# Optimization experiments

Measured on AMD Instinct MI355X. Metric: run time of the kernel, lower is better.

The kernel has to match this reference:

```python
import jax, jax.numpy as jnp
import numpy as np

TEMPERATURE = 0.5
EPS = 1e-8  # F.cosine_similarity eps


def _neg_mask_indices(B):
    # mask: ones, zero diagonal, zero the two positive off-diagonals
    N = 2 * B
    mask = np.ones((N, N), dtype=bool)
    np.fill_diagonal(mask, False)
    idx = np.arange(B)
    mask[idx, idx + B] = False
    mask[idx + B, idx] = False
    rows, cols = np.nonzero(mask)  # static, computed at trace time
    return rows, cols


def setup_inputs() -> dict:
    key = jax.random.key(0)
    k1, k2 = jax.random.split(key)
    B, D = 4096, 128
    z_i = jax.random.normal(k1, (B, D), dtype=jnp.float32)
    z_j = jax.random.normal(k2, (B, D), dtype=jnp.float32)
    return {"z_i": z_i, "z_j": z_j}


def reference(z_i, z_j):
    B = z_i.shape[0]
    N = 2 * B
    z = jnp.concatenate([z_i, z_j], axis=0)  # [N, D]
    norm = jnp.maximum(jnp.linalg.norm(z, axis=1, keepdims=True), EPS)
    zn = z / norm
    sim = (zn @ zn.T) / TEMPERATURE  # [N, N] cosine similarity / temp

    # positives: the i <-> i+B pairs
    sim_i_j = jnp.diagonal(sim, offset=B)
    sim_j_i = jnp.diagonal(sim, offset=-B)
    positives = jnp.concatenate([sim_i_j, sim_j_i], axis=0)[:, None]  # [N, 1]

    rows, cols = _neg_mask_indices(B)
    negatives = sim[rows, cols].reshape(N, N - 2)  # [N, N-2]

    logits = jnp.concatenate([positives, negatives], axis=1)  # [N, N-1]
    # cross-entropy with labels == 0 (positive is column 0)
    loss = jnp.mean(jax.nn.logsumexp(logits, axis=1) - logits[:, 0])
    return loss
```

## Files before the change

### kernel.cpp

```cpp
#include <hip/hip_runtime.h>
#include <hip/hip_bf16.h>
#include <math.h>


typedef __attribute__((ext_vector_type(8))) short bf16x8;
typedef __attribute__((ext_vector_type(4))) float f32x4;

#define NROWS 8192
#define DDIM  128
#define BHALF 4096
#define CHUNK 32
#define TILE  128
#define NT    64
#define NBLK  2080
#define CPAD  128
#define SQRT_E2S 1.6986435980707531f
#define TWO_LN2  1.3862943611198906f
#define LN2      0.6931471805599453f
#define EXPDIAG  7.38905609893065f

static __device__ __forceinline__ unsigned short f2bf(float f) {
  unsigned int u = __float_as_uint(f);
  unsigned int r = (u + 0x7fffu + ((u >> 16) & 1u)) >> 16;
  return (unsigned short)r;
}

static __device__ __forceinline__ void glds16(const unsigned short* g, unsigned short* l) {
  __builtin_amdgcn_global_load_lds((const __attribute__((address_space(1))) unsigned int*)g,
                                   (__attribute__((address_space(3))) unsigned int*)l,
                                   16, 0, 0);
}

__global__ void norm_kernel(const float* __restrict__ zi, const float* __restrict__ zj,
                            unsigned short* __restrict__ zn,
                            float* __restrict__ pos, float* __restrict__ out) {
  __shared__ float2 xbuf[2][64];
  int wave = threadIdx.x >> 6;
  int lane = threadIdx.x & 63;
  int pi   = blockIdx.x * 2 + (wave & 1);
  int row  = pi + (wave >> 1) * BHALF;
  const float* src = (row < BHALF) ? (zi + (size_t)row * DDIM)
                                   : (zj + (size_t)(row - BHALF) * DDIM);
  float2 v = *(const float2*)(src + 2 * lane);
  float ss = v.x * v.x + v.y * v.y;
  #pragma unroll
  for (int off = 1; off < 64; off <<= 1) ss += __shfl_xor(ss, off);
  float scale = SQRT_E2S / fmaxf(sqrtf(ss), 1e-8f);
  v.x *= scale; v.y *= scale;
  unsigned int lo = f2bf(v.x), hi = f2bf(v.y);
  ((unsigned int*)(zn + (size_t)row * DDIM))[lane] = lo | (hi << 16);

  if (wave >= 2) xbuf[wave - 2][lane] = v;
  __syncthreads();
  if (wave < 2) {
    float2 w = xbuf[wave][lane];
    float d = v.x * w.x + v.y * w.y;
    #pragma unroll
    for (int off = 1; off < 64; off <<= 1) d += __shfl_xor(d, off);
    if (lane == 0) pos[pi] = d;
  }
  if (blockIdx.x == 0 && threadIdx.x == 0) out[0] = 0.0f;
}

__global__ __launch_bounds__(256, 2)
void sim_kernel(const unsigned short* __restrict__ zn, float* __restrict__ part) {
  __shared__ unsigned short lds[4 * CHUNK * DDIM];
  __shared__ float colpart[16][CPAD];

  int t = blockIdx.x;
  int tx = (int)((129.0f - sqrtf((float)(16641 - 8 * t))) * 0.5f);
  while ((tx + 1) * NT - ((tx + 1) * tx) / 2 <= t) ++tx;
  while (tx * NT - (tx * (tx - 1)) / 2 > t) --tx;
  const int ty = t - (tx * NT - (tx * (tx - 1)) / 2) + tx;
  const bool diag = (tx == ty);

  const int wave = threadIdx.x >> 6;
  const int lane = threadIdx.x & 63;
  const int l15  = lane & 15;
  const int quad = lane >> 4;

  const int row_base = tx * TILE + wave * 32;
  const int col_base = ty * TILE;

  bf16x8 a[2][4];
  const unsigned short* abase = zn + (size_t)(row_base + l15) * DDIM + quad * 8;
  #pragma unroll
  for (int mi = 0; mi < 2; ++mi)
    #pragma unroll
    for (int kf = 0; kf < 4; ++kf)
      a[mi][kf] = *(const bf16x8*)(abase + mi * 16 * DDIM + kf * 32);
  __builtin_amdgcn_sched_barrier(0);

  const int t0 = wave * 64 + lane;
  const int r0 = t0 >> 4,         c0 = (t0 & 15) ^ (r0 & 15);
  const int r1 = (t0 + 256) >> 4, c1 = (t0 & 15) ^ (r1 & 15);
  const unsigned short* gst0 = zn + (size_t)(col_base + r0) * DDIM + c0 * 8;
  const unsigned short* gst1 = zn + (size_t)(col_base + r1) * DDIM + c1 * 8;
  #pragma unroll
  for (int ch = 0; ch < 4; ++ch) {
    glds16(gst0 + (size_t)ch * CHUNK * DDIM, lds + ch * 4096 + wave * 512);
    glds16(gst1 + (size_t)ch * CHUNK * DDIM, lds + ch * 4096 + 2048 + wave * 512);
  }
  __builtin_amdgcn_sched_barrier(0);

  int rdoff[4];
  #pragma unroll
  for (int kf = 0; kf < 4; ++kf)
    rdoff[kf] = l15 * DDIM + (((quad + 4 * kf) ^ l15) << 3);

  float rs[2][4];
  #pragma unroll
  for (int mi = 0; mi < 2; ++mi)
    #pragma unroll
    for (int r = 0; r < 4; ++r) rs[mi][r] = 0.0f;

  float* cp = &colpart[wave * 4 + quad][l15];

#define SIM_PHASE(CH, VM)                                                      \
  {                                                                            \
    asm volatile("s_waitcnt vmcnt(" VM ")" ::: "memory");                      \
    __builtin_amdgcn_s_barrier();                                              \
    __builtin_amdgcn_sched_barrier(0);                                         \
    const unsigned short* lb = lds + (CH) * 4096;                              \
    _Pragma("unroll")                                                          \
    for (int ni = 0; ni < 2; ++ni) {                                           \
      bf16x8 b[4];                                                             \
      _Pragma("unroll")                                                        \
      for (int kf = 0; kf < 4; ++kf)                                           \
        b[kf] = *(const bf16x8*)(lb + ni * 16 * DDIM + rdoff[kf]);             \
      f32x4 acc[2];                                                            \
      __builtin_amdgcn_s_setprio(1);                                           \
      _Pragma("unroll")                                                        \
      for (int mi = 0; mi < 2; ++mi) {                                         \
        f32x4 z = {0.0f, 0.0f, 0.0f, 0.0f};                                    \
        acc[mi] = __builtin_amdgcn_mfma_f32_16x16x32_bf16(a[mi][0], b[0], z, 0, 0, 0); \
      }                                                                        \
      _Pragma("unroll")                                                        \
      for (int kf = 1; kf < 4; ++kf)                                           \
        _Pragma("unroll")                                                      \
        for (int mi = 0; mi < 2; ++mi)                                         \
          acc[mi] = __builtin_amdgcn_mfma_f32_16x16x32_bf16(a[mi][kf], b[kf], acc[mi], 0, 0, 0); \
      __builtin_amdgcn_s_setprio(0);                                           \
      float cs = 0.0f;                                                         \
      _Pragma("unroll")                                                        \
      for (int mi = 0; mi < 2; ++mi)                                           \
        _Pragma("unroll")                                                      \
        for (int r = 0; r < 4; ++r) {                                          \
          float e = __builtin_amdgcn_exp2f(acc[mi][r]);                        \
          rs[mi][r] += e;                                                      \
          cs += e;                                                             \
        }                                                                      \
      cp[((CH) * 2 + ni) * 16] = cs;                                           \
    }                                                                          \
  }

  SIM_PHASE(0, "6")
  SIM_PHASE(1, "4")
  SIM_PHASE(2, "2")
  SIM_PHASE(3, "0")
#undef SIM_PHASE

  #pragma unroll
  for (int mi = 0; mi < 2; ++mi)
    #pragma unroll
    for (int r = 0; r < 4; ++r) {
      float v = rs[mi][r];
      v += __shfl_xor(v, 1);
      v += __shfl_xor(v, 2);
      v += __shfl_xor(v, 4);
      v += __shfl_xor(v, 8);
      if (l15 == 0)
        part[(size_t)ty * NROWS + row_base + mi * 16 + quad * 4 + r] = v;
    }
  __syncthreads();
  if (!diag && threadIdx.x < TILE) {
    float v = 0.0f;
    #pragma unroll
    for (int s = 0; s < 16; ++s) v += colpart[s][threadIdx.x];
    part[(size_t)tx * NROWS + col_base + threadIdx.x] = v;
  }
}

__global__ void finalize_kernel(const float* __restrict__ part,
                                const float* __restrict__ pos,
                                float* __restrict__ out) {
  __shared__ float red[4];
  int r = blockIdx.x * 256 + threadIdx.x;
  float s = 0.0f;
  #pragma unroll 16
  for (int k = 0; k < NT; ++k) s += part[(size_t)k * NROWS + r];
  float v = logf(s - EXPDIAG) - LN2 * pos[r & (BHALF - 1)];
  #pragma unroll
  for (int off = 1; off < 64; off <<= 1) v += __shfl_xor(v, off);
  int wave = threadIdx.x >> 6, lane = threadIdx.x & 63;
  if (lane == 0) red[wave] = v;
  __syncthreads();
  if (threadIdx.x == 0)
    atomicAdd(out, (red[0] + red[1] + red[2] + red[3]) * (1.0f / 8192.0f));
}

extern "C" void kernel_launch(void* const* d_in, const int* in_sizes, int n_in,
                              void* d_out, int out_size, void* d_ws, size_t ws_size,
                              hipStream_t stream) {
  const float* zi = (const float*)d_in[0];
  const float* zj = (const float*)d_in[1];
  char* ws = (char*)d_ws;
  unsigned short* zn = (unsigned short*)ws;
  float* part = (float*)(ws + (size_t)NROWS * DDIM * 2);
  float* pos  = (float*)(ws + (size_t)NROWS * DDIM * 2
                            + (size_t)NT * NROWS * 4);
  float* out = (float*)d_out;

  norm_kernel<<<2048, 256, 0, stream>>>(zi, zj, zn, pos, out);
  sim_kernel<<<NBLK, 256, 0, stream>>>(zn, part);
  finalize_kernel<<<32, 256, 0, stream>>>(part, pos, out);
}
```

Baseline: 81.18 us.

## Process two column tiles per sim block, prefetch second tile, widen finalize

Each sim block now handles two adjacent upper-triangle column tiles, reusing the A-fragment register loads across both. The second tile's loads into LDS are issued right after the first tile's compute finishes. This halves the grid (1056 blocks) and raises launch bounds to 4 blocks per CU. The finalize kernel splits each row's 64-partial sum across two thread halves and uses 64 blocks, to get more memory parallelism. Risks: the second tile's load overlaps only with the column-partial reduction, so much of its latency may stay exposed. The higher occupancy target may also force register spills.

Result: no change. 81.06 us (-0.2%).

```diff
diff --git a/kernel.cpp b/kernel.cpp
--- a/kernel.cpp
+++ b/kernel.cpp
@@ -12,10 +12,9 @@
 #define CHUNK 32
 #define TILE  128
 #define NT    64
-#define NBLK  2080
+#define NBLKP 1056
 #define CPAD  128
 #define SQRT_E2S 1.6986435980707531f
-#define TWO_LN2  1.3862943611198906f
 #define LN2      0.6931471805599453f
 #define EXPDIAG  7.38905609893065f
 
@@ -29,6 +28,12 @@
   __builtin_amdgcn_global_load_lds((const __attribute__((address_space(1))) unsigned int*)g,
                                    (__attribute__((address_space(3))) unsigned int*)l,
                                    16, 0, 0);
+}
+
+static __device__ __forceinline__ int pfx(int x) {
+  int u = x >> 1;
+  int base = u * (65 - u);
+  return (x & 1) ? base + (32 - u) : base;
 }
 
 __global__ void norm_kernel(const float* __restrict__ zi, const float* __restrict__ zj,
@@ -62,17 +67,18 @@
   if (blockIdx.x == 0 && threadIdx.x == 0) out[0] = 0.0f;
 }
 
-__global__ __launch_bounds__(256, 2)
+__global__ __launch_bounds__(256, 4)
 void sim_kernel(const unsigned short* __restrict__ zn, float* __restrict__ part) {
   __shared__ unsigned short lds[4 * CHUNK * DDIM];
   __shared__ float colpart[16][CPAD];
 
-  int t = blockIdx.x;
-  int tx = (int)((129.0f - sqrtf((float)(16641 - 8 * t))) * 0.5f);
-  while ((tx + 1) * NT - ((tx + 1) * tx) / 2 <= t) ++tx;
-  while (tx * NT - (tx * (tx - 1)) / 2 > t) --tx;
-  const int ty = t - (tx * NT - (tx * (tx - 1)) / 2) + tx;
-  const bool diag = (tx == ty);
+  int bid = blockIdx.x;
+  int tx = (int)(65.0f - sqrtf(fmaxf(0.0f, 4225.0f - 4.0f * (float)bid)));
+  tx = tx < 0 ? 0 : (tx > 63 ? 63 : tx);
+  while (pfx(tx + 1) <= bid) ++tx;
+  while (pfx(tx) > bid) --tx;
+  const int ty0  = tx + 2 * (bid - pfx(tx));
+  const bool has2 = (ty0 + 1) < NT;
 
   const int wave = threadIdx.x >> 6;
   const int lane = threadIdx.x & 63;
@@ -80,7 +86,6 @@
   const int quad = lane >> 4;
 
   const int row_base = tx * TILE + wave * 32;
-  const int col_base = ty * TILE;
 
   bf16x8 a[2][4];
   const unsigned short* abase = zn + (size_t)(row_base + l15) * DDIM + quad * 8;
@@ -94,12 +99,17 @@
   const int t0 = wave * 64 + lane;
   const int r0 = t0 >> 4,         c0 = (t0 & 15) ^ (r0 & 15);
   const int r1 = (t0 + 256) >> 4, c1 = (t0 & 15) ^ (r1 & 15);
-  const unsigned short* gst0 = zn + (size_t)(col_base + r0) * DDIM + c0 * 8;
-  const unsigned short* gst1 = zn + (size_t)(col_base + r1) * DDIM + c1 * 8;
-  #pragma unroll
-  for (int ch = 0; ch < 4; ++ch) {
-    glds16(gst0 + (size_t)ch * CHUNK * DDIM, lds + ch * 4096 + wave * 512);
-    glds16(gst1 + (size_t)ch * CHUNK * DDIM, lds + ch * 4096 + 2048 + wave * 512);
+  const size_t goff0 = (size_t)r0 * DDIM + c0 * 8;
+  const size_t goff1 = (size_t)r1 * DDIM + c1 * 8;
+
+  {
+    const unsigned short* g0 = zn + (size_t)(ty0 * TILE) * DDIM + goff0;
+    const unsigned short* g1 = zn + (size_t)(ty0 * TILE) * DDIM + goff1;
+    #pragma unroll
+    for (int ch = 0; ch < 4; ++ch) {
+      glds16(g0 + (size_t)ch * CHUNK * DDIM, lds + ch * 4096 + wave * 512);
+      glds16(g1 + (size_t)ch * CHUNK * DDIM, lds + ch * 4096 + 2048 + wave * 512);
+    }
   }
   __builtin_amdgcn_sched_barrier(0);
 
@@ -107,12 +117,6 @@
   #pragma unroll
   for (int kf = 0; kf < 4; ++kf)
     rdoff[kf] = l15 * DDIM + (((quad + 4 * kf) ^ l15) << 3);
-
-  float rs[2][4];
-  #pragma unroll
-  for (int mi = 0; mi < 2; ++mi)
-    #pragma unroll
-    for (int r = 0; r < 4; ++r) rs[mi][r] = 0.0f;
 
   float* cp = &colpart[wave * 4 + quad][l15];
 
@@ -154,49 +158,85 @@
     }                                                                          \
   }
 
-  SIM_PHASE(0, "6")
-  SIM_PHASE(1, "4")
-  SIM_PHASE(2, "2")
-  SIM_PHASE(3, "0")
+  for (int tile = 0; tile < 2; ++tile) {
+    const int ty = ty0 + tile;
+    const bool diag = (ty == tx);
+    const int col_base = ty * TILE;
+
+    float rs[2][4];
+    #pragma unroll
+    for (int mi = 0; mi < 2; ++mi)
+      #pragma unroll
+      for (int r = 0; r < 4; ++r) rs[mi][r] = 0.0f;
+
+    SIM_PHASE(0, "6")
+    SIM_PHASE(1, "4")
+    SIM_PHASE(2, "2")
+    SIM_PHASE(3, "0")
+
+    #pragma unroll
+    for (int mi = 0; mi < 2; ++mi)
+      #pragma unroll
+      for (int r = 0; r < 4; ++r) {
+        float v = rs[mi][r];
+        v += __shfl_xor(v, 1);
+        v += __shfl_xor(v, 2);
+        v += __shfl_xor(v, 4);
+        v += __shfl_xor(v, 8);
+        if (l15 == 0)
+          part[(size_t)ty * NROWS + row_base + mi * 16 + quad * 4 + r] = v;
+      }
+
+    __syncthreads();
+
+    if (tile == 0 && has2) {
+      const unsigned short* g0 = zn + (size_t)((ty0 + 1) * TILE) * DDIM + goff0;
+      const unsigned short* g1 = zn + (size_t)((ty0 + 1) * TILE) * DDIM + goff1;
+      #pragma unroll
+      for (int ch = 0; ch < 4; ++ch) {
+        glds16(g0 + (size_t)ch * CHUNK * DDIM, lds + ch * 4096 + wave * 512);
+        glds16(g1 + (size_t)ch * CHUNK * DDIM, lds + ch * 4096 + 2048 + wave * 512);
+      }
+    }
+
+    if (!diag && threadIdx.x < TILE) {
+      float v = 0.0f;
+      #pragma unroll
+      for (int s = 0; s < 16; ++s) v += colpart[s][threadIdx.x];
+      part[(size_t)tx * NROWS + col_base + threadIdx.x] = v;
+    }
+
+    if (!has2) break;
+  }
 #undef SIM_PHASE
-
-  #pragma unroll
-  for (int mi = 0; mi < 2; ++mi)
-    #pragma unroll
-    for (int r = 0; r < 4; ++r) {
-      float v = rs[mi][r];
-      v += __shfl_xor(v, 1);
-      v += __shfl_xor(v, 2);
-      v += __shfl_xor(v, 4);
-      v += __shfl_xor(v, 8);
-      if (l15 == 0)
-        part[(size_t)ty * NROWS + row_base + mi * 16 + quad * 4 + r] = v;
-    }
-  __syncthreads();
-  if (!diag && threadIdx.x < TILE) {
-    float v = 0.0f;
-    #pragma unroll
-    for (int s = 0; s < 16; ++s) v += colpart[s][threadIdx.x];
-    part[(size_t)tx * NROWS + col_base + threadIdx.x] = v;
-  }
 }
 
 __global__ void finalize_kernel(const float* __restrict__ part,
                                 const float* __restrict__ pos,
                                 float* __restrict__ out) {
-  __shared__ float red[4];
-  int r = blockIdx.x * 256 + threadIdx.x;
+  __shared__ float fsum[128];
+  __shared__ float red[2];
+  int rloc = threadIdx.x & 127;
+  int half = threadIdx.x >> 7;
+  int r = blockIdx.x * 128 + rloc;
   float s = 0.0f;
-  #pragma unroll 16
-  for (int k = 0; k < NT; ++k) s += part[(size_t)k * NROWS + r];
-  float v = logf(s - EXPDIAG) - LN2 * pos[r & (BHALF - 1)];
-  #pragma unroll
-  for (int off = 1; off < 64; off <<= 1) v += __shfl_xor(v, off);
-  int wave = threadIdx.x >> 6, lane = threadIdx.x & 63;
-  if (lane == 0) red[wave] = v;
+  #pragma unroll 8
+  for (int k = half * 32; k < half * 32 + 32; ++k)
+    s += part[(size_t)k * NROWS + r];
+  if (half == 0) fsum[rloc] = s;
+  __syncthreads();
+  if (half == 1) fsum[rloc] += s;
+  __syncthreads();
+  if (threadIdx.x < 128) {
+    float tot = fsum[threadIdx.x];
+    float v = logf(tot - EXPDIAG) - LN2 * pos[r & (BHALF - 1)];
+    #pragma unroll
+    for (int off = 1; off < 64; off <<= 1) v += __shfl_xor(v, off);
+    if ((threadIdx.x & 63) == 0) red[threadIdx.x >> 6] = v;
+  }
   __syncthreads();
   if (threadIdx.x == 0)
-    atomicAdd(out, (red[0] + red[1] + red[2] + red[3]) * (1.0f / 8192.0f));
+    atomicAdd(out, (red[0] + red[1]) * (1.0f / 8192.0f));
 }
 
 extern "C" void kernel_launch(void* const* d_in, const int* in_sizes, int n_in,
@@ -212,6 +252,6 @@
   float* out = (float*)d_out;
 
   norm_kernel<<<2048, 256, 0, stream>>>(zi, zj, zn, pos, out);
-  sim_kernel<<<NBLK, 256, 0, stream>>>(zn, part);
-  finalize_kernel<<<32, 256, 0, stream>>>(part, pos, out);
-}
+  sim_kernel<<<NBLKP, 256, 0, stream>>>(zn, part);
+  finalize_kernel<<<64, 256, 0, stream>>>(part, pos, out);
+}
```

## Replace symmetric triangular tiling with full row strips and pipelined column chunks

Applied to the files above, without the earlier changes.

Drops the upper-triangular tile schedule that exploited symmetry of the similarity matrix and instead has each block compute a 128x512 strip of the full matrix. It streams 16 column chunks through a 4-slot LDS ring buffer with refills after each phase, removes the column-sum LDS reduction, raises occupancy to 4 blocks per CU, and removes the s_setprio priority hints around the MFMA block. This doubles the matmul and exp work in exchange for simpler reductions and deeper load pipelining; finalize sums 16 partials instead of 64.

Result: slower. 142.5 us (+75.6%).

```diff
diff --git a/kernel.cpp b/kernel.cpp
--- a/kernel.cpp
+++ b/kernel.cpp
@@ -11,11 +11,10 @@
 #define BHALF 4096
 #define CHUNK 32
 #define TILE  128
-#define NT    64
-#define NBLK  2080
-#define CPAD  128
+#define NCG   16
+#define CGSZ  512
+#define NCHUNK 16
 #define SQRT_E2S 1.6986435980707531f
-#define TWO_LN2  1.3862943611198906f
 #define LN2      0.6931471805599453f
 #define EXPDIAG  7.38905609893065f
 
@@ -62,25 +61,19 @@
   if (blockIdx.x == 0 && threadIdx.x == 0) out[0] = 0.0f;
 }
 
-__global__ __launch_bounds__(256, 2)
+__global__ __launch_bounds__(256, 4)
 void sim_kernel(const unsigned short* __restrict__ zn, float* __restrict__ part) {
   __shared__ unsigned short lds[4 * CHUNK * DDIM];
-  __shared__ float colpart[16][CPAD];
-
-  int t = blockIdx.x;
-  int tx = (int)((129.0f - sqrtf((float)(16641 - 8 * t))) * 0.5f);
-  while ((tx + 1) * NT - ((tx + 1) * tx) / 2 <= t) ++tx;
-  while (tx * NT - (tx * (tx - 1)) / 2 > t) --tx;
-  const int ty = t - (tx * NT - (tx * (tx - 1)) / 2) + tx;
-  const bool diag = (tx == ty);
-
-  const int wave = threadIdx.x >> 6;
-  const int lane = threadIdx.x & 63;
-  const int l15  = lane & 15;
-  const int quad = lane >> 4;
-
-  const int row_base = tx * TILE + wave * 32;
-  const int col_base = ty * TILE;
+
+  const int strip = blockIdx.x >> 4;
+  const int cg    = blockIdx.x & 15;
+  const int wave  = threadIdx.x >> 6;
+  const int lane  = threadIdx.x & 63;
+  const int l15   = lane & 15;
+  const int quad  = lane >> 4;
+
+  const int row_base = strip * TILE + wave * 32;
+  const int col0     = cg * CGSZ;
 
   bf16x8 a[2][4];
   const unsigned short* abase = zn + (size_t)(row_base + l15) * DDIM + quad * 8;
@@ -94,8 +87,9 @@
   const int t0 = wave * 64 + lane;
   const int r0 = t0 >> 4,         c0 = (t0 & 15) ^ (r0 & 15);
   const int r1 = (t0 + 256) >> 4, c1 = (t0 & 15) ^ (r1 & 15);
-  const unsigned short* gst0 = zn + (size_t)(col_base + r0) * DDIM + c0 * 8;
-  const unsigned short* gst1 = zn + (size_t)(col_base + r1) * DDIM + c1 * 8;
+  const unsigned short* gst0 = zn + (size_t)(col0 + r0) * DDIM + c0 * 8;
+  const unsigned short* gst1 = zn + (size_t)(col0 + r1) * DDIM + c1 * 8;
+
   #pragma unroll
   for (int ch = 0; ch < 4; ++ch) {
     glds16(gst0 + (size_t)ch * CHUNK * DDIM, lds + ch * 4096 + wave * 512);
@@ -114,14 +108,12 @@
     #pragma unroll
     for (int r = 0; r < 4; ++r) rs[mi][r] = 0.0f;
 
-  float* cp = &colpart[wave * 4 + quad][l15];
-
 #define SIM_PHASE(CH, VM)                                                      \
   {                                                                            \
     asm volatile("s_waitcnt vmcnt(" VM ")" ::: "memory");                      \
     __builtin_amdgcn_s_barrier();                                              \
     __builtin_amdgcn_sched_barrier(0);                                         \
-    const unsigned short* lb = lds + (CH) * 4096;                              \
+    const unsigned short* lb = lds + ((CH) & 3) * 4096;                        \
     _Pragma("unroll")                                                          \
     for (int ni = 0; ni < 2; ++ni) {                                           \
       bf16x8 b[4];                                                             \
@@ -129,7 +121,6 @@
       for (int kf = 0; kf < 4; ++kf)                                           \
         b[kf] = *(const bf16x8*)(lb + ni * 16 * DDIM + rdoff[kf]);             \
       f32x4 acc[2];                                                            \
-      __builtin_amdgcn_s_setprio(1);                                           \
       _Pragma("unroll")                                                        \
       for (int mi = 0; mi < 2; ++mi) {                                         \
         f32x4 z = {0.0f, 0.0f, 0.0f, 0.0f};                                    \
@@ -140,24 +131,26 @@
         _Pragma("unroll")                                                      \
         for (int mi = 0; mi < 2; ++mi)                                         \
           acc[mi] = __builtin_amdgcn_mfma_f32_16x16x32_bf16(a[mi][kf], b[kf], acc[mi], 0, 0, 0); \
-      __builtin_amdgcn_s_setprio(0);                                           \
-      float cs = 0.0f;                                                         \
       _Pragma("unroll")                                                        \
       for (int mi = 0; mi < 2; ++mi)                                           \
         _Pragma("unroll")                                                      \
-        for (int r = 0; r < 4; ++r) {                                          \
-          float e = __builtin_amdgcn_exp2f(acc[mi][r]);                        \
-          rs[mi][r] += e;                                                      \
-          cs += e;                                                             \
-        }                                                                      \
-      cp[((CH) * 2 + ni) * 16] = cs;                                           \
+        for (int r = 0; r < 4; ++r)                                            \
+          rs[mi][r] += __builtin_amdgcn_exp2f(acc[mi][r]);                     \
+    }                                                                          \
+    __builtin_amdgcn_sched_barrier(0);                                         \
+    __builtin_amdgcn_s_barrier();                                              \
+    if ((CH) + 4 < NCHUNK) {                                                   \
+      glds16(gst0 + (size_t)((CH) + 4) * CHUNK * DDIM,                         \
+             lds + ((CH) & 3) * 4096 + wave * 512);                            \
+      glds16(gst1 + (size_t)((CH) + 4) * CHUNK * DDIM,                         \
+             lds + ((CH) & 3) * 4096 + 2048 + wave * 512);                     \
     }                                                                          \
   }
 
-  SIM_PHASE(0, "6")
-  SIM_PHASE(1, "4")
-  SIM_PHASE(2, "2")
-  SIM_PHASE(3, "0")
+  SIM_PHASE(0,  "6")  SIM_PHASE(1,  "6")  SIM_PHASE(2,  "6")  SIM_PHASE(3,  "6")
+  SIM_PHASE(4,  "6")  SIM_PHASE(5,  "6")  SIM_PHASE(6,  "6")  SIM_PHASE(7,  "6")
+  SIM_PHASE(8,  "6")  SIM_PHASE(9,  "6")  SIM_PHASE(10, "6")  SIM_PHASE(11, "6")
+  SIM_PHASE(12, "6")  SIM_PHASE(13, "4")  SIM_PHASE(14, "2")  SIM_PHASE(15, "0")
 #undef SIM_PHASE
 
   #pragma unroll
@@ -170,15 +163,8 @@
       v += __shfl_xor(v, 4);
       v += __shfl_xor(v, 8);
       if (l15 == 0)
-        part[(size_t)ty * NROWS + row_base + mi * 16 + quad * 4 + r] = v;
+        part[(size_t)cg * NROWS + row_base + mi * 16 + quad * 4 + r] = v;
     }
-  __syncthreads();
-  if (!diag && threadIdx.x < TILE) {
-    float v = 0.0f;
-    #pragma unroll
-    for (int s = 0; s < 16; ++s) v += colpart[s][threadIdx.x];
-    part[(size_t)tx * NROWS + col_base + threadIdx.x] = v;
-  }
 }
 
 __global__ void finalize_kernel(const float* __restrict__ part,
@@ -187,8 +173,8 @@
   __shared__ float red[4];
   int r = blockIdx.x * 256 + threadIdx.x;
   float s = 0.0f;
-  #pragma unroll 16
-  for (int k = 0; k < NT; ++k) s += part[(size_t)k * NROWS + r];
+  #pragma unroll
+  for (int k = 0; k < NCG; ++k) s += part[(size_t)k * NROWS + r];
   float v = logf(s - EXPDIAG) - LN2 * pos[r & (BHALF - 1)];
   #pragma unroll
   for (int off = 1; off < 64; off <<= 1) v += __shfl_xor(v, off);
@@ -208,10 +194,10 @@
   unsigned short* zn = (unsigned short*)ws;
   float* part = (float*)(ws + (size_t)NROWS * DDIM * 2);
   float* pos  = (float*)(ws + (size_t)NROWS * DDIM * 2
-                            + (size_t)NT * NROWS * 4);
+                            + (size_t)NCG * NROWS * 4);
   float* out = (float*)d_out;
 
   norm_kernel<<<2048, 256, 0, stream>>>(zi, zj, zn, pos, out);
-  sim_kernel<<<NBLK, 256, 0, stream>>>(zn, part);
+  sim_kernel<<<1024, 256, 0, stream>>>(zn, part);
   finalize_kernel<<<32, 256, 0, stream>>>(part, pos, out);
 }
```
